# Performance work log

Measured on AMD Instinct MI355X. Metric: run time of the kernel, lower is better.

Reference implementation:

```python
import jax, jax.numpy as jnp
import numpy as np

MARGIN = 1.0
EPS = 1e-05
B = 8192
D = 128
NUM_CLASSES = 256


def setup_inputs() -> dict:
    key = jax.random.key(0)
    k1, k2 = jax.random.split(key)
    feature = jax.random.normal(k1, (B, D), dtype=jnp.float32)
    label = jax.random.randint(k2, (B,), 0, NUM_CLASSES, dtype=jnp.int32)
    return {"feature": feature, "label": label}


def reference(feature, label):
    # Pairwise Euclidean distance matrix: ||x_i||^2 + ||x_j||^2 - 2 x_i.x_j + eps, then sqrt
    sq = jnp.sum(feature * feature, axis=1, keepdims=True)  # [B, 1]
    dist = jnp.sqrt(jnp.maximum(sq + sq.T - 2.0 * (feature @ feature.T) + EPS, 0.0))  # [B, B]

    same = label[:, None] == label[None, :]  # [B, B] bool, includes self on diagonal
    inf = jnp.array(jnp.inf, dtype=dist.dtype)

    # Original sorts each row and takes same[1]: the SECOND smallest same-label distance
    # (the smallest is the anchor itself, distance sqrt(eps)).
    d_same = jnp.where(same, dist, inf)
    two_smallest = -jax.lax.top_k(-d_same, 2)[0]  # [B, 2], ascending smallest two
    pos = two_smallest[:, 1]  # nearest positive excluding self

    # diff.min(): hardest (closest) negative per row
    neg = jnp.min(jnp.where(same, inf, dist), axis=1)

    hinge = jnp.maximum(MARGIN + pos - neg, 0.0)
    return jnp.mean(hinge)
```

## Files before the change

kernel.cpp:

```cpp
#include <hip/hip_runtime.h>
#include <math.h>


#define BN 8192
#define MARGIN_F 1.0f
#define EPS_F 1e-5f

typedef __attribute__((ext_vector_type(8))) short short8;
typedef __attribute__((ext_vector_type(4))) float floatx4;

__device__ __forceinline__ unsigned short bf16_rne(float x, float& r) {
    unsigned u = __float_as_uint(x);
    u += 0x7FFF + ((u >> 16) & 1);
    unsigned short h = (unsigned short)(u >> 16);
    r = __uint_as_float(((unsigned)h) << 16);
    return h;
}

__global__ __launch_bounds__(256) void prep_kernel(const float* __restrict__ f,
                                                   short8* __restrict__ fbT,
                                                   float* __restrict__ sq,
                                                   float* __restrict__ g_acc,
                                                   unsigned* __restrict__ counter) {
    int gid = blockIdx.x * 256 + threadIdx.x;
    if (gid == 0) { *g_acc = 0.f; *counter = 0u; }
    int row = gid >> 2, part = gid & 3;
    const float4* f4 = (const float4*)f + (size_t)row * 32 + part * 8;
    float s = 0.f;
#pragma unroll
    for (int cc = 0; cc < 4; ++cc) {
        float4 v0 = f4[cc * 2], v1 = f4[cc * 2 + 1];
        float r0, r1, r2, r3, r4, r5, r6, r7;
        short8 o;
        o[0] = (short)bf16_rne(v0.x, r0);
        o[1] = (short)bf16_rne(v0.y, r1);
        o[2] = (short)bf16_rne(v0.z, r2);
        o[3] = (short)bf16_rne(v0.w, r3);
        o[4] = (short)bf16_rne(v1.x, r4);
        o[5] = (short)bf16_rne(v1.y, r5);
        o[6] = (short)bf16_rne(v1.z, r6);
        o[7] = (short)bf16_rne(v1.w, r7);
        fbT[(size_t)(part * 4 + cc) * BN + row] = o;
        s += r0 * r0 + r1 * r1 + r2 * r2 + r3 * r3 +
             r4 * r4 + r5 * r5 + r6 * r6 + r7 * r7;
    }
    s += __shfl_xor(s, 1, 4);
    s += __shfl_xor(s, 2, 4);
    if (part == 0) sq[row] = s;
}

__device__ __forceinline__ void stage_tile(const short8* __restrict__ fbT,
                                           short8* buf, int j0, int wv, int lane) {
#pragma unroll
    for (int it = 0; it < 8; ++it) {
        int cb = wv * 512 + it * 64;
        int kc = cb >> 7, r0 = cb & 127;
        const short8* g = fbT + ((size_t)kc * BN + j0 + r0 + lane);
        __builtin_amdgcn_global_load_lds(
            (const __attribute__((address_space(1))) void*)g,
            (__attribute__((address_space(3))) void*)(buf + cb),
            16, 0, 0);
    }
}

__global__ __launch_bounds__(256, 2) void main_kernel(const short8* __restrict__ fbT,
                                                      const int* __restrict__ lbl,
                                                      const float* __restrict__ sq,
                                                      float4* __restrict__ part) {
    __shared__ short8 Bs0[2048];
    __shared__ short8 Bs1[2048];
    __shared__ float4 mrg[128];

    const int t = threadIdx.x;
    const int lane = t & 63;
    const int wv = t >> 6;
    const int wm = wv >> 1;
    const int wn = wv & 1;
    const int q = lane >> 4, c = lane & 15;
    const int i0 = blockIdx.x * 128;
    const int jb = blockIdx.y * 1024;

    stage_tile(fbT, Bs0, jb, wv, lane);

    short8 a[4][4];
#pragma unroll
    for (int mf = 0; mf < 4; ++mf) {
        int row = i0 + wm * 64 + mf * 16 + c;
#pragma unroll
        for (int ks = 0; ks < 4; ++ks)
            a[mf][ks] = fbT[(size_t)(ks * 4 + q) * BN + row];
    }
    int li[4][4];
#pragma unroll
    for (int mf = 0; mf < 4; ++mf)
#pragma unroll
        for (int rg = 0; rg < 4; ++rg)
            li[mf][rg] = lbl[i0 + wm * 64 + mf * 16 + q * 4 + rg];

    float s1[4][4], s2[4][4], n1[4][4];
#pragma unroll
    for (int mf = 0; mf < 4; ++mf)
#pragma unroll
        for (int rg = 0; rg < 4; ++rg) {
            s1[mf][rg] = INFINITY; s2[mf][rg] = INFINITY; n1[mf][rg] = INFINITY;
        }

    __syncthreads();

#pragma unroll
    for (int jt = 0; jt < 8; ++jt) {
        short8* cur = (jt & 1) ? Bs1 : Bs0;
        short8* nxt = (jt & 1) ? Bs0 : Bs1;
        const int j0 = jb + jt * 128;
        if (jt < 7) stage_tile(fbT, nxt, j0 + 128, wv, lane);

        int ljv[4]; float sjv[4];
#pragma unroll
        for (int nf = 0; nf < 4; ++nf) {
            int jc = j0 + wn * 64 + nf * 16 + c;
            ljv[nf] = lbl[jc];
            sjv[nf] = sq[jc];
        }

        floatx4 acc[4][4];
#pragma unroll
        for (int mf = 0; mf < 4; ++mf)
#pragma unroll
            for (int nf = 0; nf < 4; ++nf) acc[mf][nf] = (floatx4)0.f;

#pragma unroll
        for (int ks = 0; ks < 4; ++ks) {
            short8 b[4];
#pragma unroll
            for (int nf = 0; nf < 4; ++nf)
                b[nf] = cur[(ks * 4 + q) * 128 + wn * 64 + nf * 16 + c];
#pragma unroll
            for (int mf = 0; mf < 4; ++mf)
#pragma unroll
                for (int nf = 0; nf < 4; ++nf)
                    acc[mf][nf] = __builtin_amdgcn_mfma_f32_16x16x32_bf16(
                        a[mf][ks], b[nf], acc[mf][nf], 0, 0, 0);
        }

#pragma unroll
        for (int nf = 0; nf < 4; ++nf) {
#pragma unroll
            for (int mf = 0; mf < 4; ++mf)
#pragma unroll
                for (int rg = 0; rg < 4; ++rg) {
                    float v = fmaf(-2.0f, acc[mf][nf][rg], sjv[nf]);
                    bool same = (li[mf][rg] == ljv[nf]);
                    float vs = same ? v : INFINITY;
                    float vd = same ? INFINITY : v;
                    s2[mf][rg] = fminf(s2[mf][rg], fmaxf(s1[mf][rg], vs));
                    s1[mf][rg] = fminf(s1[mf][rg], vs);
                    n1[mf][rg] = fminf(n1[mf][rg], vd);
                }
        }
        __syncthreads();
    }

#pragma unroll
    for (int m = 1; m < 16; m <<= 1) {
#pragma unroll
        for (int mf = 0; mf < 4; ++mf)
#pragma unroll
            for (int rg = 0; rg < 4; ++rg) {
                float o1 = __shfl_xor(s1[mf][rg], m, 16);
                float o2 = __shfl_xor(s2[mf][rg], m, 16);
                float on = __shfl_xor(n1[mf][rg], m, 16);
                float lo = fminf(s1[mf][rg], o1);
                float hi = fminf(fmaxf(s1[mf][rg], o1), fminf(s2[mf][rg], o2));
                s1[mf][rg] = lo; s2[mf][rg] = hi;
                n1[mf][rg] = fminf(n1[mf][rg], on);
            }
    }

    if (c == 0 && wn == 1) {
#pragma unroll
        for (int mf = 0; mf < 4; ++mf)
#pragma unroll
            for (int rg = 0; rg < 4; ++rg) {
                int row = wm * 64 + mf * 16 + q * 4 + rg;
                mrg[row] = make_float4(s1[mf][rg], s2[mf][rg], n1[mf][rg], 0.f);
            }
    }
    __syncthreads();
    if (c == 0 && wn == 0) {
#pragma unroll
        for (int mf = 0; mf < 4; ++mf)
#pragma unroll
            for (int rg = 0; rg < 4; ++rg) {
                int row = wm * 64 + mf * 16 + q * 4 + rg;
                float4 o = mrg[row];
                float a1 = s1[mf][rg], a2 = s2[mf][rg];
                float lo = fminf(a1, o.x);
                float hi = fminf(fmaxf(a1, o.x), fminf(a2, o.y));
                float nn = fminf(n1[mf][rg], o.z);
                part[blockIdx.y * BN + i0 + row] = make_float4(lo, hi, nn, 0.f);
            }
    }
}

__global__ __launch_bounds__(128) void merge_kernel(const float4* __restrict__ part,
                                                    const float* __restrict__ sq,
                                                    float* __restrict__ g_acc,
                                                    unsigned* __restrict__ counter,
                                                    float* __restrict__ out) {
    int r = blockIdx.x * 128 + threadIdx.x;
    float s1 = INFINITY, s2v = INFINITY, n = INFINITY;
#pragma unroll
    for (int k = 0; k < 8; ++k) {
        float4 pp = part[k * BN + r];
        float lo = fminf(s1, pp.x);
        float hi = fminf(fmaxf(s1, pp.x), fminf(s2v, pp.y));
        s1 = lo; s2v = hi;
        n = fminf(n, pp.z);
    }
    float si = sq[r];
    float pos = sqrtf(fmaxf(si + s2v + EPS_F, 0.f));
    float neg = sqrtf(fmaxf(si + n + EPS_F, 0.f));
    float h = fmaxf(MARGIN_F + pos - neg, 0.f);
    __shared__ float red[2];
#pragma unroll
    for (int m = 32; m >= 1; m >>= 1) h += __shfl_down(h, m, 64);
    if ((threadIdx.x & 63) == 0) red[threadIdx.x >> 6] = h;
    __syncthreads();
    if (threadIdx.x == 0) {
        atomicAdd(g_acc, red[0] + red[1]);
        __threadfence();
        unsigned old = atomicAdd(counter, 1u);
        if (old == 63u) {
            float tot = atomicAdd(g_acc, 0.0f);
            out[0] = tot / (float)BN;
        }
    }
}

extern "C" void kernel_launch(void* const* d_in, const int* in_sizes, int n_in,
                              void* d_out, int out_size, void* d_ws, size_t ws_size,
                              hipStream_t stream) {
    const float* f = (const float*)d_in[0];
    const int* lbl = (const int*)d_in[1];
    float* sq = (float*)d_ws;
    short8* fbT = (short8*)((char*)d_ws + 32768);
    float4* part = (float4*)((char*)d_ws + 32768 + 2097152);
    float* g_acc = (float*)((char*)d_ws + 32768 + 2097152 + 1048576);
    unsigned* counter = (unsigned*)(g_acc + 1);
    float* out = (float*)d_out;

    prep_kernel<<<128, 256, 0, stream>>>(f, fbT, sq, g_acc, counter);
    main_kernel<<<dim3(64, 8), 256, 0, stream>>>(fbT, lbl, sq, part);
    merge_kernel<<<64, 128, 0, stream>>>(part, sq, g_acc, counter, out);
}
```

Baseline: 102.3 us.

## Drop LDS staging; each wave loads its B fragments directly from global

```diff
diff --git a/kernel.cpp b/kernel.cpp
--- a/kernel.cpp
+++ b/kernel.cpp
@@ -49,43 +49,21 @@
     if (part == 0) sq[row] = s;
 }
 
-__device__ __forceinline__ void stage_tile(const short8* __restrict__ fbT,
-                                           short8* buf, int j0, int wv, int lane) {
-#pragma unroll
-    for (int it = 0; it < 8; ++it) {
-        int cb = wv * 512 + it * 64;
-        int kc = cb >> 7, r0 = cb & 127;
-        const short8* g = fbT + ((size_t)kc * BN + j0 + r0 + lane);
-        __builtin_amdgcn_global_load_lds(
-            (const __attribute__((address_space(1))) void*)g,
-            (__attribute__((address_space(3))) void*)(buf + cb),
-            16, 0, 0);
-    }
-}
-
 __global__ __launch_bounds__(256, 2) void main_kernel(const short8* __restrict__ fbT,
                                                       const int* __restrict__ lbl,
                                                       const float* __restrict__ sq,
                                                       float4* __restrict__ part) {
-    __shared__ short8 Bs0[2048];
-    __shared__ short8 Bs1[2048];
-    __shared__ float4 mrg[128];
-
     const int t = threadIdx.x;
     const int lane = t & 63;
     const int wv = t >> 6;
-    const int wm = wv >> 1;
-    const int wn = wv & 1;
     const int q = lane >> 4, c = lane & 15;
-    const int i0 = blockIdx.x * 128;
-    const int jb = blockIdx.y * 1024;
-
-    stage_tile(fbT, Bs0, jb, wv, lane);
+    const int i0 = blockIdx.x * 256 + wv * 64;
+    const int jb = blockIdx.y * 512;
 
     short8 a[4][4];
 #pragma unroll
     for (int mf = 0; mf < 4; ++mf) {
-        int row = i0 + wm * 64 + mf * 16 + c;
+        int row = i0 + mf * 16 + c;
 #pragma unroll
         for (int ks = 0; ks < 4; ++ks)
             a[mf][ks] = fbT[(size_t)(ks * 4 + q) * BN + row];
@@ -95,7 +73,7 @@
     for (int mf = 0; mf < 4; ++mf)
 #pragma unroll
         for (int rg = 0; rg < 4; ++rg)
-            li[mf][rg] = lbl[i0 + wm * 64 + mf * 16 + q * 4 + rg];
+            li[mf][rg] = lbl[i0 + mf * 16 + q * 4 + rg];
 
     float s1[4][4], s2[4][4], n1[4][4];
 #pragma unroll
@@ -105,19 +83,21 @@
             s1[mf][rg] = INFINITY; s2[mf][rg] = INFINITY; n1[mf][rg] = INFINITY;
         }
 
-    __syncthreads();
-
-#pragma unroll
+#pragma unroll 2
     for (int jt = 0; jt < 8; ++jt) {
-        short8* cur = (jt & 1) ? Bs1 : Bs0;
-        short8* nxt = (jt & 1) ? Bs0 : Bs1;
-        const int j0 = jb + jt * 128;
-        if (jt < 7) stage_tile(fbT, nxt, j0 + 128, wv, lane);
+        const int j0 = jb + jt * 64;
+
+        short8 b[4][4];
+#pragma unroll
+        for (int ks = 0; ks < 4; ++ks)
+#pragma unroll
+            for (int nf = 0; nf < 4; ++nf)
+                b[ks][nf] = fbT[(size_t)(ks * 4 + q) * BN + j0 + nf * 16 + c];
 
         int ljv[4]; float sjv[4];
 #pragma unroll
         for (int nf = 0; nf < 4; ++nf) {
-            int jc = j0 + wn * 64 + nf * 16 + c;
+            int jc = j0 + nf * 16 + c;
             ljv[nf] = lbl[jc];
             sjv[nf] = sq[jc];
         }
@@ -129,18 +109,13 @@
             for (int nf = 0; nf < 4; ++nf) acc[mf][nf] = (floatx4)0.f;
 
 #pragma unroll
-        for (int ks = 0; ks < 4; ++ks) {
-            short8 b[4];
-#pragma unroll
-            for (int nf = 0; nf < 4; ++nf)
-                b[nf] = cur[(ks * 4 + q) * 128 + wn * 64 + nf * 16 + c];
+        for (int ks = 0; ks < 4; ++ks)
 #pragma unroll
             for (int mf = 0; mf < 4; ++mf)
 #pragma unroll
                 for (int nf = 0; nf < 4; ++nf)
                     acc[mf][nf] = __builtin_amdgcn_mfma_f32_16x16x32_bf16(
-                        a[mf][ks], b[nf], acc[mf][nf], 0, 0, 0);
-        }
+                        a[mf][ks], b[ks][nf], acc[mf][nf], 0, 0, 0);
 
 #pragma unroll
         for (int nf = 0; nf < 4; ++nf) {
@@ -157,7 +132,6 @@
                     n1[mf][rg] = fminf(n1[mf][rg], vd);
                 }
         }
-        __syncthreads();
     }
 
 #pragma unroll
@@ -176,28 +150,14 @@
             }
     }
 
-    if (c == 0 && wn == 1) {
+    if (c == 0) {
 #pragma unroll
         for (int mf = 0; mf < 4; ++mf)
 #pragma unroll
             for (int rg = 0; rg < 4; ++rg) {
-                int row = wm * 64 + mf * 16 + q * 4 + rg;
-                mrg[row] = make_float4(s1[mf][rg], s2[mf][rg], n1[mf][rg], 0.f);
-            }
-    }
-    __syncthreads();
-    if (c == 0 && wn == 0) {
-#pragma unroll
-        for (int mf = 0; mf < 4; ++mf)
-#pragma unroll
-            for (int rg = 0; rg < 4; ++rg) {
-                int row = wm * 64 + mf * 16 + q * 4 + rg;
-                float4 o = mrg[row];
-                float a1 = s1[mf][rg], a2 = s2[mf][rg];
-                float lo = fminf(a1, o.x);
-                float hi = fminf(fmaxf(a1, o.x), fminf(a2, o.y));
-                float nn = fminf(n1[mf][rg], o.z);
-                part[blockIdx.y * BN + i0 + row] = make_float4(lo, hi, nn, 0.f);
+                int row = i0 + mf * 16 + q * 4 + rg;
+                part[blockIdx.y * BN + row] =
+                    make_float4(s1[mf][rg], s2[mf][rg], n1[mf][rg], 0.f);
             }
     }
 }
@@ -210,7 +170,7 @@
     int r = blockIdx.x * 128 + threadIdx.x;
     float s1 = INFINITY, s2v = INFINITY, n = INFINITY;
 #pragma unroll
-    for (int k = 0; k < 8; ++k) {
+    for (int k = 0; k < 16; ++k) {
         float4 pp = part[k * BN + r];
         float lo = fminf(s1, pp.x);
         float hi = fminf(fmaxf(s1, pp.x), fminf(s2v, pp.y));
@@ -245,11 +205,11 @@
     float* sq = (float*)d_ws;
     short8* fbT = (short8*)((char*)d_ws + 32768);
     float4* part = (float4*)((char*)d_ws + 32768 + 2097152);
-    float* g_acc = (float*)((char*)d_ws + 32768 + 2097152 + 1048576);
+    float* g_acc = (float*)((char*)d_ws + 32768 + 2097152 + 2097152);
     unsigned* counter = (unsigned*)(g_acc + 1);
     float* out = (float*)d_out;
 
     prep_kernel<<<128, 256, 0, stream>>>(f, fbT, sq, g_acc, counter);
-    main_kernel<<<dim3(64, 8), 256, 0, stream>>>(fbT, lbl, sq, part);
+    main_kernel<<<dim3(32, 16), 256, 0, stream>>>(fbT, lbl, sq, part);
     merge_kernel<<<64, 128, 0, stream>>>(part, sq, g_acc, counter, out);
 }
```

Result: faster. 93.39 us (-8.7%).
